# Performance work log

Measured on AMD Instinct MI355X. Metric: run time of the kernel, lower is better.

The kernel has to match this reference:

```python
import jax, jax.numpy as jnp
import numpy as np


def _gcn_conv(x, W, b, src, dst, num_nodes):
    # x: [N, F_in], W: [F_in, F_out], b: [F_out]
    # src/dst already include self-loops. Symmetric normalization per PyG GCNConv.
    ones = jnp.ones(src.shape[0], dtype=x.dtype)
    deg = jax.ops.segment_sum(ones, dst, num_segments=num_nodes)  # in-degree w/ self-loops
    dinv = jnp.where(deg > 0, jax.lax.rsqrt(deg), 0.0)
    norm = dinv[src] * dinv[dst]                                  # [E]
    h = x @ W                                                     # [N, F_out]
    msg = h[src] * norm[:, None]                                  # gather + scale
    out = jax.ops.segment_sum(msg, dst, num_segments=num_nodes)   # scatter-add
    return out + b


def setup_inputs() -> dict:
    key = jax.random.key(0)
    k1, k2, k3, k4, k5, k6 = jax.random.split(key, 6)
    N, E = 1000000, 4000000
    x = jax.random.normal(k1, (N, 4), dtype=jnp.float32)
    edge_index = jax.random.randint(k2, (2, E), 0, N, dtype=jnp.int64)
    W1 = jax.random.normal(k3, (4, 16), dtype=jnp.float32) * 0.5
    b1 = jax.random.normal(k4, (16,), dtype=jnp.float32) * 0.1
    W2 = jax.random.normal(k5, (16, 2), dtype=jnp.float32) * 0.25
    b2 = jax.random.normal(k6, (2,), dtype=jnp.float32) * 0.1
    return {"x": x, "edge_index": edge_index, "num_nodes": N,
            "W1": W1, "b1": b1, "W2": W2, "b2": b2}


def reference(x, edge_index, num_nodes, W1, b1, W2, b2):
    # Add self-loops once (GCNConv default add_self_loops=True)
    loop = jnp.arange(num_nodes, dtype=edge_index.dtype)
    src = jnp.concatenate([edge_index[0], loop])
    dst = jnp.concatenate([edge_index[1], loop])
    h = jax.nn.relu(_gcn_conv(x, W1, b1, src, dst, num_nodes))
    h = _gcn_conv(h, W2, b2, src, dst, num_nodes)
    return jax.nn.log_softmax(h, axis=1)
```

## Files before the change

### kernel.cpp

```cpp
#include <hip/hip_runtime.h>


typedef unsigned int u32;

#define BSHIFT 11
#define BNODES 2048
#define MAXBINS 2048
#define EPB 16384

__device__ __forceinline__ u32 pack_bf16(float a, float b) {
    u32 ua = __float_as_uint(a), ub = __float_as_uint(b);
    ua += 0x7FFFu + ((ua >> 16) & 1u);
    ub += 0x7FFFu + ((ub >> 16) & 1u);
    return (ua >> 16) | (ub & 0xFFFF0000u);
}
__device__ __forceinline__ float bf_lo(u32 p) { return __uint_as_float(p << 16); }
__device__ __forceinline__ float bf_hi(u32 p) { return __uint_as_float(p & 0xFFFF0000u); }

__device__ __forceinline__ u32 src_quarter(u32 sv, u32 Q1, u32 Q2, u32 Q3) {
    return (sv >= Q2) ? ((sv >= Q3) ? 3u : 2u) : ((sv >= Q1) ? 1u : 0u);
}

__global__ void k_bincount(const int* __restrict__ src, const int* __restrict__ dst,
                           int E, int NBINS, u32 Q1, u32 Q2, u32 Q3,
                           u32* __restrict__ binTotal, u32* __restrict__ bh) {
    __shared__ u32 h[MAXBINS];
    const int tid = threadIdx.x;
    for (int j = tid; j < MAXBINS; j += 256) h[j] = 0;
    __syncthreads();
    const int start = blockIdx.x * EPB;
    const int end = min(start + EPB, E);
    for (int e = start + tid; e < end; e += 256) {
        u32 d = (u32)dst[e];
        u32 b = ((d >> BSHIFT) << 2) | src_quarter((u32)src[e], Q1, Q2, Q3);
        atomicAdd(&h[b], 1u);
    }
    __syncthreads();
    u32* bhrow = bh + (size_t)blockIdx.x * MAXBINS;
    for (int j = tid; j < NBINS; j += 256) {
        u32 c = h[j];
        bhrow[j] = c;
        if (c) atomicAdd(&binTotal[j], c);
    }
}

__global__ void k_binscan(const u32* __restrict__ binTotal,
                          u32* __restrict__ binBase,
                          u32* __restrict__ cursor, int NBINS, int E) {
    __shared__ u32 s[1024];
    const int tid = threadIdx.x;
    const int i0 = 2 * tid, i1 = 2 * tid + 1;
    u32 v0 = (i0 < NBINS) ? binTotal[i0] : 0u;
    u32 v1 = (i1 < NBINS) ? binTotal[i1] : 0u;
    u32 p = v0 + v1;
    s[tid] = p;
    __syncthreads();
    for (int d = 1; d < 1024; d <<= 1) {
        u32 t = (tid >= d) ? s[tid - d] : 0u;
        __syncthreads();
        s[tid] += t;
        __syncthreads();
    }
    u32 excl = s[tid] - p;
    if (i0 < NBINS) { binBase[i0] = excl;      cursor[i0] = excl; }
    if (i1 < NBINS) { binBase[i1] = excl + v0; cursor[i1] = excl + v0; }
    if (tid == 0) binBase[NBINS] = (u32)E;
}

__global__ void k_binscatter(const int* __restrict__ src, const int* __restrict__ dst,
                             int E, int NBINS, u32 Q1, u32 Q2, u32 Q3,
                             u32* __restrict__ cursor,
                             const u32* __restrict__ bh, u32* __restrict__ rec) {
    __shared__ u32 h[MAXBINS];
    const int tid = threadIdx.x;
    const u32* bhrow = bh + (size_t)blockIdx.x * MAXBINS;
    for (int j = tid; j < MAXBINS; j += 256) h[j] = 0;
    __syncthreads();
    for (int j = tid; j < NBINS; j += 256) {
        u32 c = bhrow[j];
        if (c) h[j] = atomicAdd(&cursor[j], c);
    }
    __syncthreads();
    const int start = blockIdx.x * EPB;
    const int end = min(start + EPB, E);
    for (int e = start + tid; e < end; e += 256) {
        u32 d = (u32)dst[e];
        u32 sv = (u32)src[e];
        u32 b = ((d >> BSHIFT) << 2) | src_quarter(sv, Q1, Q2, Q3);
        u32 slot = atomicAdd(&h[b], 1u);
        rec[slot] = sv | ((d & (BNODES - 1u)) << 20);
    }
}

__global__ void k_deg(const u32* __restrict__ rec, const u32* __restrict__ binBase,
                      const float4* __restrict__ x,
                      float* __restrict__ dinv, uint2* __restrict__ xd, int N) {
    __shared__ u32 deg[BNODES];
    const int tid = threadIdx.x;
    const int b = blockIdx.x;
    for (int j = tid; j < BNODES; j += 512) deg[j] = 0;
    __syncthreads();
    const u32 s0 = binBase[4 * b], s1 = binBase[4 * b + 4];
    for (u32 i = s0 + tid; i < s1; i += 512)
        atomicAdd(&deg[rec[i] >> 20], 1u);
    __syncthreads();
    const int nodeBase = b << BSHIFT;
    for (int n = tid; n < BNODES; n += 512) {
        int gn = nodeBase + n;
        if (gn < N) {
            float d = rsqrtf((float)(deg[n] + 1u));
            dinv[gn] = d;
            float4 xi = x[gn];
            xd[gn] = make_uint2(pack_bf16(xi.x * d, xi.y * d),
                                pack_bf16(xi.z * d, xi.w * d));
        }
    }
}

__global__ void k_l1(const u32* __restrict__ rec, const u32* __restrict__ binBase,
                     const float* __restrict__ dinv, const uint2* __restrict__ xd,
                     const float* __restrict__ W1, const float* __restrict__ b1,
                     const float* __restrict__ W2,
                     u32* __restrict__ h2, int N) {
    __shared__ float agg[BNODES * 4];
    const int tid = threadIdx.x;
    const int b = blockIdx.x;
    for (int j = tid; j < BNODES * 4; j += 1024) agg[j] = 0.f;
    __syncthreads();
    const u32 s0 = binBase[4 * b], s1 = binBase[4 * b + 4];
    const u32 T = 1024;

#define L1_ACC(R, V) do {                                 \
        float* p = &agg[((R) >> 20) * 4];                 \
        atomicAdd(p + 0, bf_lo((V).x));                   \
        atomicAdd(p + 1, bf_hi((V).x));                   \
        atomicAdd(p + 2, bf_lo((V).y));                   \
        atomicAdd(p + 3, bf_hi((V).y));                   \
    } while (0)

    u32 i = s0 + tid;
    for (; i + 3 * T < s1; i += 4 * T) {
        u32 r0 = rec[i], r1 = rec[i + T], r2 = rec[i + 2 * T], r3 = rec[i + 3 * T];
        uint2 v0 = xd[r0 & 0xFFFFFu];
        uint2 v1 = xd[r1 & 0xFFFFFu];
        uint2 v2 = xd[r2 & 0xFFFFFu];
        uint2 v3 = xd[r3 & 0xFFFFFu];
        L1_ACC(r0, v0); L1_ACC(r1, v1); L1_ACC(r2, v2); L1_ACC(r3, v3);
    }
    for (; i < s1; i += T) {
        u32 r = rec[i];
        uint2 v = xd[r & 0xFFFFFu];
        L1_ACC(r, v);
    }
#undef L1_ACC
    __syncthreads();

    const int nodeBase = b << BSHIFT;
    for (int n = tid; n < BNODES; n += 1024) {
        int gn = nodeBase + n;
        if (gn >= N) continue;
        float di = dinv[gn];
        uint2 xs = xd[gn];
        float ax = (bf_lo(xs.x) + agg[n * 4 + 0]) * di;
        float ay = (bf_hi(xs.x) + agg[n * 4 + 1]) * di;
        float az = (bf_lo(xs.y) + agg[n * 4 + 2]) * di;
        float aw = (bf_hi(xs.y) + agg[n * 4 + 3]) * di;
        float g0 = 0.f, g1 = 0.f;
#pragma unroll
        for (int k = 0; k < 16; ++k) {
            float h = ax * W1[k] + ay * W1[16 + k] + az * W1[32 + k] + aw * W1[48 + k] + b1[k];
            h = fmaxf(h, 0.f);
            g0 += h * W2[2 * k];
            g1 += h * W2[2 * k + 1];
        }
        h2[gn] = pack_bf16(g0 * di, g1 * di);
    }
}

__global__ void k_l2(const u32* __restrict__ rec, const u32* __restrict__ binBase,
                     const float* __restrict__ dinv, const u32* __restrict__ h2,
                     const float* __restrict__ b2, float2* __restrict__ out, int N) {
    __shared__ float agg[BNODES * 2];
    const int tid = threadIdx.x;
    const int b = blockIdx.x;
    for (int j = tid; j < BNODES * 2; j += 1024) agg[j] = 0.f;
    __syncthreads();
    const u32 s0 = binBase[4 * b], s1 = binBase[4 * b + 4];
    const u32 T = 1024;

#define L2_ACC(R, V) do {                                 \
        float* p = &agg[((R) >> 20) * 2];                 \
        atomicAdd(p + 0, bf_lo(V));                       \
        atomicAdd(p + 1, bf_hi(V));                       \
    } while (0)

    u32 i = s0 + tid;
    for (; i + 7 * T < s1; i += 8 * T) {
        u32 r0 = rec[i],         r1 = rec[i + T],     r2 = rec[i + 2 * T], r3 = rec[i + 3 * T];
        u32 r4 = rec[i + 4 * T], r5 = rec[i + 5 * T], r6 = rec[i + 6 * T], r7 = rec[i + 7 * T];
        u32 v0 = h2[r0 & 0xFFFFFu], v1 = h2[r1 & 0xFFFFFu];
        u32 v2 = h2[r2 & 0xFFFFFu], v3 = h2[r3 & 0xFFFFFu];
        u32 v4 = h2[r4 & 0xFFFFFu], v5 = h2[r5 & 0xFFFFFu];
        u32 v6 = h2[r6 & 0xFFFFFu], v7 = h2[r7 & 0xFFFFFu];
        L2_ACC(r0, v0); L2_ACC(r1, v1); L2_ACC(r2, v2); L2_ACC(r3, v3);
        L2_ACC(r4, v4); L2_ACC(r5, v5); L2_ACC(r6, v6); L2_ACC(r7, v7);
    }
    for (; i < s1; i += T) {
        u32 r = rec[i];
        u32 v = h2[r & 0xFFFFFu];
        L2_ACC(r, v);
    }
#undef L2_ACC
    __syncthreads();

    const int nodeBase = b << BSHIFT;
    for (int n = tid; n < BNODES; n += 1024) {
        int gn = nodeBase + n;
        if (gn >= N) continue;
        float di = dinv[gn];
        u32 self = h2[gn];
        float g0 = (bf_lo(self) + agg[n * 2 + 0]) * di + b2[0];
        float g1 = (bf_hi(self) + agg[n * 2 + 1]) * di + b2[1];
        float m = fmaxf(g0, g1);
        float l = m + logf(expf(g0 - m) + expf(g1 - m));
        out[gn] = make_float2(g0 - l, g1 - l);
    }
}

extern "C" void kernel_launch(void* const* d_in, const int* in_sizes, int n_in,
                              void* d_out, int out_size, void* d_ws, size_t ws_size,
                              hipStream_t stream) {
    const float* x  = (const float*)d_in[0];
    const int*   ei = (const int*)d_in[1];
    const float* W1 = (const float*)d_in[3];
    const float* b1 = (const float*)d_in[4];
    const float* W2 = (const float*)d_in[5];
    const float* b2 = (const float*)d_in[6];

    const int N = in_sizes[0] / 4;
    const int E = in_sizes[1] / 2;
    const int* src = ei;
    const int* dst = ei + E;
    const int NB = (N + BNODES - 1) >> BSHIFT;
    const int NBINS = 4 * NB;
    const u32 Q1 = (u32)(N >> 2), Q2 = (u32)(N >> 1), Q3 = (u32)(3 * (N >> 2));
    const int gA = (E + EPB - 1) / EPB;

    char* w = (char*)d_ws;
    u32*   rec  = (u32*)(w);
    float* dinv = (float*)(w + 4 * (size_t)E);
    uint2* xd   = (uint2*)(w + 4 * (size_t)E + 4 * (size_t)N);
    u32*   h2   = (u32*)(w + 4 * (size_t)E + 12 * (size_t)N);
    u32*   meta = (u32*)(w + 4 * (size_t)E + 16 * (size_t)N);
    u32*   binTotal = meta;
    u32*   binBase  = meta + MAXBINS;
    u32*   cursor   = meta + 2 * MAXBINS + 1;
    u32*   bh       = meta + 3 * MAXBINS + 2;

    hipMemsetAsync(binTotal, 0, sizeof(u32) * (size_t)NBINS, stream);
    k_bincount<<<gA, 256, 0, stream>>>(src, dst, E, NBINS, Q1, Q2, Q3, binTotal, bh);
    k_binscan<<<1, 1024, 0, stream>>>(binTotal, binBase, cursor, NBINS, E);
    k_binscatter<<<gA, 256, 0, stream>>>(src, dst, E, NBINS, Q1, Q2, Q3, cursor, bh, rec);
    k_deg<<<NB, 512, 0, stream>>>(rec, binBase, (const float4*)x, dinv, xd, N);
    k_l1<<<NB, 1024, 0, stream>>>(rec, binBase, dinv, xd, W1, b1, W2, h2, N);
    k_l2<<<NB, 1024, 0, stream>>>(rec, binBase, dinv, h2, b2, (float2*)d_out, N);
}
```

Before: 323.8 us.

## Shrink destination bins to 1024 nodes and drop source-quarter sub-binning

Halves the destination bin size to 1024 nodes, which doubles the number of aggregation blocks (about 977). It removes the four-way source-range sub-binning used to give the gathers locality, so the bincount and scatter passes read only dst for counting and the scan works on one value per thread. The aggregation kernels now run with 512 threads and an 8-way unrolled gather loop. In exchange, source gathers within a bin are no longer grouped by source range, which may hurt L2 locality. With 1024 nodes per bin, the rec format leaves only 10 bits for the local index, so the 20-bit source field still fits.

```diff
diff --git a/kernel.cpp b/kernel.cpp
--- a/kernel.cpp
+++ b/kernel.cpp
@@ -3,9 +3,9 @@
 
 typedef unsigned int u32;
 
-#define BSHIFT 11
-#define BNODES 2048
-#define MAXBINS 2048
+#define BSHIFT 10
+#define BNODES 1024
+#define MAXBINS 1024
 #define EPB 16384
 
 __device__ __forceinline__ u32 pack_bf16(float a, float b) {
@@ -17,12 +17,7 @@
 __device__ __forceinline__ float bf_lo(u32 p) { return __uint_as_float(p << 16); }
 __device__ __forceinline__ float bf_hi(u32 p) { return __uint_as_float(p & 0xFFFF0000u); }
 
-__device__ __forceinline__ u32 src_quarter(u32 sv, u32 Q1, u32 Q2, u32 Q3) {
-    return (sv >= Q2) ? ((sv >= Q3) ? 3u : 2u) : ((sv >= Q1) ? 1u : 0u);
-}
-
-__global__ void k_bincount(const int* __restrict__ src, const int* __restrict__ dst,
-                           int E, int NBINS, u32 Q1, u32 Q2, u32 Q3,
+__global__ void k_bincount(const int* __restrict__ dst, int E, int NBINS,
                            u32* __restrict__ binTotal, u32* __restrict__ bh) {
     __shared__ u32 h[MAXBINS];
     const int tid = threadIdx.x;
@@ -30,11 +25,8 @@
     __syncthreads();
     const int start = blockIdx.x * EPB;
     const int end = min(start + EPB, E);
-    for (int e = start + tid; e < end; e += 256) {
-        u32 d = (u32)dst[e];
-        u32 b = ((d >> BSHIFT) << 2) | src_quarter((u32)src[e], Q1, Q2, Q3);
-        atomicAdd(&h[b], 1u);
-    }
+    for (int e = start + tid; e < end; e += 256)
+        atomicAdd(&h[((u32)dst[e]) >> BSHIFT], 1u);
     __syncthreads();
     u32* bhrow = bh + (size_t)blockIdx.x * MAXBINS;
     for (int j = tid; j < NBINS; j += 256) {
@@ -49,11 +41,8 @@
                           u32* __restrict__ cursor, int NBINS, int E) {
     __shared__ u32 s[1024];
     const int tid = threadIdx.x;
-    const int i0 = 2 * tid, i1 = 2 * tid + 1;
-    u32 v0 = (i0 < NBINS) ? binTotal[i0] : 0u;
-    u32 v1 = (i1 < NBINS) ? binTotal[i1] : 0u;
-    u32 p = v0 + v1;
-    s[tid] = p;
+    u32 v = (tid < NBINS) ? binTotal[tid] : 0u;
+    s[tid] = v;
     __syncthreads();
     for (int d = 1; d < 1024; d <<= 1) {
         u32 t = (tid >= d) ? s[tid - d] : 0u;
@@ -61,15 +50,13 @@
         s[tid] += t;
         __syncthreads();
     }
-    u32 excl = s[tid] - p;
-    if (i0 < NBINS) { binBase[i0] = excl;      cursor[i0] = excl; }
-    if (i1 < NBINS) { binBase[i1] = excl + v0; cursor[i1] = excl + v0; }
+    u32 excl = s[tid] - v;
+    if (tid < NBINS) { binBase[tid] = excl; cursor[tid] = excl; }
     if (tid == 0) binBase[NBINS] = (u32)E;
 }
 
 __global__ void k_binscatter(const int* __restrict__ src, const int* __restrict__ dst,
-                             int E, int NBINS, u32 Q1, u32 Q2, u32 Q3,
-                             u32* __restrict__ cursor,
+                             int E, int NBINS, u32* __restrict__ cursor,
                              const u32* __restrict__ bh, u32* __restrict__ rec) {
     __shared__ u32 h[MAXBINS];
     const int tid = threadIdx.x;
@@ -85,10 +72,9 @@
     const int end = min(start + EPB, E);
     for (int e = start + tid; e < end; e += 256) {
         u32 d = (u32)dst[e];
-        u32 sv = (u32)src[e];
-        u32 b = ((d >> BSHIFT) << 2) | src_quarter(sv, Q1, Q2, Q3);
+        u32 b = d >> BSHIFT;
         u32 slot = atomicAdd(&h[b], 1u);
-        rec[slot] = sv | ((d & (BNODES - 1u)) << 20);
+        rec[slot] = ((u32)src[e]) | ((d & (BNODES - 1u)) << 20);
     }
 }
 
@@ -100,7 +86,7 @@
     const int b = blockIdx.x;
     for (int j = tid; j < BNODES; j += 512) deg[j] = 0;
     __syncthreads();
-    const u32 s0 = binBase[4 * b], s1 = binBase[4 * b + 4];
+    const u32 s0 = binBase[b], s1 = binBase[b + 1];
     for (u32 i = s0 + tid; i < s1; i += 512)
         atomicAdd(&deg[rec[i] >> 20], 1u);
     __syncthreads();
@@ -125,10 +111,10 @@
     __shared__ float agg[BNODES * 4];
     const int tid = threadIdx.x;
     const int b = blockIdx.x;
-    for (int j = tid; j < BNODES * 4; j += 1024) agg[j] = 0.f;
-    __syncthreads();
-    const u32 s0 = binBase[4 * b], s1 = binBase[4 * b + 4];
-    const u32 T = 1024;
+    for (int j = tid; j < BNODES * 4; j += 512) agg[j] = 0.f;
+    __syncthreads();
+    const u32 s0 = binBase[b], s1 = binBase[b + 1];
+    const u32 T = 512;
 
 #define L1_ACC(R, V) do {                                 \
         float* p = &agg[((R) >> 20) * 4];                 \
@@ -139,13 +125,15 @@
     } while (0)
 
     u32 i = s0 + tid;
-    for (; i + 3 * T < s1; i += 4 * T) {
-        u32 r0 = rec[i], r1 = rec[i + T], r2 = rec[i + 2 * T], r3 = rec[i + 3 * T];
-        uint2 v0 = xd[r0 & 0xFFFFFu];
-        uint2 v1 = xd[r1 & 0xFFFFFu];
-        uint2 v2 = xd[r2 & 0xFFFFFu];
-        uint2 v3 = xd[r3 & 0xFFFFFu];
+    for (; i + 7 * T < s1; i += 8 * T) {
+        u32 r0 = rec[i],         r1 = rec[i + T],     r2 = rec[i + 2 * T], r3 = rec[i + 3 * T];
+        u32 r4 = rec[i + 4 * T], r5 = rec[i + 5 * T], r6 = rec[i + 6 * T], r7 = rec[i + 7 * T];
+        uint2 v0 = xd[r0 & 0xFFFFFu], v1 = xd[r1 & 0xFFFFFu];
+        uint2 v2 = xd[r2 & 0xFFFFFu], v3 = xd[r3 & 0xFFFFFu];
+        uint2 v4 = xd[r4 & 0xFFFFFu], v5 = xd[r5 & 0xFFFFFu];
+        uint2 v6 = xd[r6 & 0xFFFFFu], v7 = xd[r7 & 0xFFFFFu];
         L1_ACC(r0, v0); L1_ACC(r1, v1); L1_ACC(r2, v2); L1_ACC(r3, v3);
+        L1_ACC(r4, v4); L1_ACC(r5, v5); L1_ACC(r6, v6); L1_ACC(r7, v7);
     }
     for (; i < s1; i += T) {
         u32 r = rec[i];
@@ -156,7 +144,7 @@
     __syncthreads();
 
     const int nodeBase = b << BSHIFT;
-    for (int n = tid; n < BNODES; n += 1024) {
+    for (int n = tid; n < BNODES; n += 512) {
         int gn = nodeBase + n;
         if (gn >= N) continue;
         float di = dinv[gn];
@@ -183,10 +171,10 @@
     __shared__ float agg[BNODES * 2];
     const int tid = threadIdx.x;
     const int b = blockIdx.x;
-    for (int j = tid; j < BNODES * 2; j += 1024) agg[j] = 0.f;
-    __syncthreads();
-    const u32 s0 = binBase[4 * b], s1 = binBase[4 * b + 4];
-    const u32 T = 1024;
+    for (int j = tid; j < BNODES * 2; j += 512) agg[j] = 0.f;
+    __syncthreads();
+    const u32 s0 = binBase[b], s1 = binBase[b + 1];
+    const u32 T = 512;
 
 #define L2_ACC(R, V) do {                                 \
         float* p = &agg[((R) >> 20) * 2];                 \
@@ -214,7 +202,7 @@
     __syncthreads();
 
     const int nodeBase = b << BSHIFT;
-    for (int n = tid; n < BNODES; n += 1024) {
+    for (int n = tid; n < BNODES; n += 512) {
         int gn = nodeBase + n;
         if (gn >= N) continue;
         float di = dinv[gn];
@@ -242,8 +230,7 @@
     const int* src = ei;
     const int* dst = ei + E;
     const int NB = (N + BNODES - 1) >> BSHIFT;
-    const int NBINS = 4 * NB;
-    const u32 Q1 = (u32)(N >> 2), Q2 = (u32)(N >> 1), Q3 = (u32)(3 * (N >> 2));
+    const int NBINS = NB;
     const int gA = (E + EPB - 1) / EPB;
 
     char* w = (char*)d_ws;
@@ -258,10 +245,10 @@
     u32*   bh       = meta + 3 * MAXBINS + 2;
 
     hipMemsetAsync(binTotal, 0, sizeof(u32) * (size_t)NBINS, stream);
-    k_bincount<<<gA, 256, 0, stream>>>(src, dst, E, NBINS, Q1, Q2, Q3, binTotal, bh);
+    k_bincount<<<gA, 256, 0, stream>>>(dst, E, NBINS, binTotal, bh);
     k_binscan<<<1, 1024, 0, stream>>>(binTotal, binBase, cursor, NBINS, E);
-    k_binscatter<<<gA, 256, 0, stream>>>(src, dst, E, NBINS, Q1, Q2, Q3, cursor, bh, rec);
+    k_binscatter<<<gA, 256, 0, stream>>>(src, dst, E, NBINS, cursor, bh, rec);
     k_deg<<<NB, 512, 0, stream>>>(rec, binBase, (const float4*)x, dinv, xd, N);
-    k_l1<<<NB, 1024, 0, stream>>>(rec, binBase, dinv, xd, W1, b1, W2, h2, N);
-    k_l2<<<NB, 1024, 0, stream>>>(rec, binBase, dinv, h2, b2, (float2*)d_out, N);
-}
+    k_l1<<<NB, 512, 0, stream>>>(rec, binBase, dinv, xd, W1, b1, W2, h2, N);
+    k_l2<<<NB, 512, 0, stream>>>(rec, binBase, dinv, h2, b2, (float2*)d_out, N);
+}
```

Result: no change. 329.4 us (+1.7%).
